# Kernel tuning notes

Hardware: AMD Instinct MI355X
Metric: run time of the kernel (lower is better)

Reference implementation:

```python
import jax, jax.numpy as jnp
import numpy as np

N = 50000
E = 800000
D = 128


def _gcn_layer(x, row, col, ew, W, b, n):
    # PyG GCNConv (normalize=True, add_self_loops=True):
    # self-loops were already appended to row/col/ew by the caller.
    deg = jax.ops.segment_sum(ew, col, num_segments=n)          # [N]
    dis = jnp.where(deg > 0, jax.lax.rsqrt(jnp.maximum(deg, 1e-12)), 0.0)
    norm = dis[row] * ew * dis[col]                              # [E+N]
    h = x @ W                                                    # [N, D]
    msg = h[row] * norm[:, None]                                 # [E+N, D] gather-scale
    out = jax.ops.segment_sum(msg, col, num_segments=n)          # scatter-add
    return out + b


def setup_inputs() -> dict:
    key = jax.random.key(0)
    k1, k2, k3, k4, k5 = jax.random.split(key, 5)
    x = jax.random.normal(k1, (N, D), dtype=jnp.float32)
    edge_index = jax.random.randint(k2, (2, E), 0, N, dtype=jnp.int64)
    edge_weight = jax.random.uniform(k3, (E,), dtype=jnp.float32)
    s = 1.0 / np.sqrt(D)
    W1 = jax.random.uniform(k4, (D, D), minval=-s, maxval=s, dtype=jnp.float32)
    b1 = jnp.zeros((D,), dtype=jnp.float32)
    W2 = jax.random.uniform(k5, (D, D), minval=-s, maxval=s, dtype=jnp.float32)
    b2 = jnp.zeros((D,), dtype=jnp.float32)
    return {"x": x, "edge_index": edge_index, "edge_weight": edge_weight,
            "W1": W1, "b1": b1, "W2": W2, "b2": b2}


def reference(x, edge_index, edge_weight, W1, b1, W2, b2):
    n = x.shape[0]
    loop = jnp.arange(n, dtype=edge_index.dtype)
    row = jnp.concatenate([edge_index[0], loop])
    col = jnp.concatenate([edge_index[1], loop])
    ew = jnp.concatenate([edge_weight, jnp.ones((n,), dtype=edge_weight.dtype)])
    h = _gcn_layer(x, row, col, ew, W1, b1, n)
    h = jax.nn.relu(h)
    # F.dropout(training=self.training): identity in eval mode
    out = _gcn_layer(h, row, col, ew, W2, b2, n)
    return out
```

## Files before the change

### kernel.cpp

```cpp
#include <hip/hip_runtime.h>

#define NN 50000
#define NE 800000
#define DD 128

#define CAP 64
#define FIX_SCALE 16777216.0f
#define NWELEM 16384
#define GEMM_GRID ((NN + 127) / 128)

#define SHIFT2 7
#define BWID 128
#define NBUCK ((NN + BWID - 1) / BWID)
#define CAP2 2560
#define NB1 128
#define EPB ((NE + NB1 - 1) / NB1)

typedef __attribute__((ext_vector_type(8))) short short8;
typedef __attribute__((ext_vector_type(4))) float floatx4;
typedef __attribute__((ext_vector_type(4))) _Float16 half4;
typedef __attribute__((ext_vector_type(8))) _Float16 half8;


__device__ __forceinline__ void split_trunc(float x, short& hi, short& lo) {
    unsigned uh = __float_as_uint(x) >> 16;
    hi = (short)uh;
    float r = x - __uint_as_float(uh << 16);
    lo = (short)(__float_as_uint(r) >> 16);
}


__global__ void init_prep(unsigned* __restrict__ bcur,
                          const float* __restrict__ W1, const float* __restrict__ W2,
                          unsigned short* __restrict__ w1hi, unsigned short* __restrict__ w1lo,
                          unsigned short* __restrict__ w2hi, unsigned short* __restrict__ w2lo) {
    int t = blockIdx.x * blockDim.x + threadIdx.x;
    if (t < NBUCK) bcur[t] = 0u;
    int u = t - 512;
    if (u >= 0 && u < 2 * NWELEM) {
        int which = u >> 14;
        int idx = u & (NWELEM - 1);
        int k = idx >> 7, n = idx & 127;
        const float* W = which ? W2 : W1;
        unsigned short* whi = which ? w2hi : w1hi;
        unsigned short* wlo = which ? w2lo : w1lo;
        short h, l;
        split_trunc(W[idx], h, l);
        whi[n * DD + k] = (unsigned short)h;
        wlo[n * DD + k] = (unsigned short)l;
    }
}


template <bool RELU, bool SCALE, typename InT>
__device__ __forceinline__ void gemm_core(int bid, const InT* __restrict__ in,
                                          const unsigned short* __restrict__ whi,
                                          const unsigned short* __restrict__ wlo,
                                          const float* __restrict__ dis,
                                          _Float16* __restrict__ out) {
    int lane = threadIdx.x & 63;
    int wid = threadIdx.x >> 6;
    int cg = wid & 1;
    int rg = wid >> 1;
    int l16 = lane & 15;
    int quad = lane >> 4;
    int koff_base = quad * 8;

    short8 bhi[4][4], blo[4][4];
#pragma unroll
    for (int t = 0; t < 4; t++) {
        int n = cg * 64 + t * 16 + l16;
#pragma unroll
        for (int ks = 0; ks < 4; ks++) {
            int koff = ks * 32 + koff_base;
            bhi[t][ks] = *(const short8*)(whi + n * DD + koff);
            blo[t][ks] = *(const short8*)(wlo + n * DD + koff);
        }
    }

#pragma unroll
    for (int chunk = 0; chunk < 4; chunk++) {
        int base = bid * 128 + chunk * 32 + rg * 16;
        int m = base + l16;
        int mld = (m < NN) ? m : 0;
        const InT* xr = in + (size_t)mld * DD;

        short8 ahi[4], alo[4];
#pragma unroll
        for (int ks = 0; ks < 4; ks++) {
            int koff = ks * 32 + koff_base;
            float v[8];
            if constexpr (sizeof(InT) == 4) {
                float4 a0 = *(const float4*)(xr + koff);
                float4 a1 = *(const float4*)(xr + koff + 4);
                v[0] = a0.x; v[1] = a0.y; v[2] = a0.z; v[3] = a0.w;
                v[4] = a1.x; v[5] = a1.y; v[6] = a1.z; v[7] = a1.w;
            } else {
                half8 a = *(const half8*)(xr + koff);
#pragma unroll
                for (int j = 0; j < 8; j++) v[j] = (float)a[j];
            }
#pragma unroll
            for (int j = 0; j < 8; j++) {
                float xv = RELU ? fmaxf(v[j], 0.0f) : v[j];
                short h, l;
                split_trunc(xv, h, l);
                ahi[ks][j] = h;
                alo[ks][j] = l;
            }
        }

        floatx4 acc[4];
#pragma unroll
        for (int t = 0; t < 4; t++) acc[t] = (floatx4)(0.0f);

#pragma unroll
        for (int ks = 0; ks < 4; ks++) {
#pragma unroll
            for (int t = 0; t < 4; t++) {
                acc[t] = __builtin_amdgcn_mfma_f32_16x16x32_bf16(ahi[ks], bhi[t][ks], acc[t], 0, 0, 0);
                acc[t] = __builtin_amdgcn_mfma_f32_16x16x32_bf16(alo[ks], bhi[t][ks], acc[t], 0, 0, 0);
                acc[t] = __builtin_amdgcn_mfma_f32_16x16x32_bf16(ahi[ks], blo[t][ks], acc[t], 0, 0, 0);
            }
        }

#pragma unroll
        for (int r = 0; r < 4; r++) {
            int rowm = base + quad * 4 + r;
            if (rowm < NN) {
                float dsc = SCALE ? dis[rowm] : 1.0f;
                _Float16* o = out + (size_t)rowm * DD + cg * 64 + l16;
#pragma unroll
                for (int t = 0; t < 4; t++) o[t * 16] = (_Float16)(acc[t][r] * dsc);
            }
        }
    }
}


__device__ __forceinline__ void scatter_core(int bid, const int* __restrict__ row,
                                             const int* __restrict__ col,
                                             const float* __restrict__ ew,
                                             unsigned* __restrict__ bcur,
                                             uint2* __restrict__ staged) {
    __shared__ unsigned cnt1[NBUCK];
    __shared__ unsigned base1[NBUCK];

    for (int k = threadIdx.x; k < NBUCK; k += 256) cnt1[k] = 0u;
    __syncthreads();

    int e0 = bid * EPB;
    int e1 = min(e0 + EPB, NE);

    for (int e = e0 + (int)threadIdx.x; e < e1; e += 256) {
        atomicAdd(&cnt1[col[e] >> SHIFT2], 1u);
    }
    __syncthreads();

    for (int k = threadIdx.x; k < NBUCK; k += 256) {
        unsigned n = cnt1[k];
        base1[k] = n ? atomicAdd(&bcur[k], n) : 0u;
        cnt1[k] = 0u;
    }
    __syncthreads();

    for (int e = e0 + (int)threadIdx.x; e < e1; e += 256) {
        int c = col[e];
        int bk = c >> SHIFT2;
        unsigned r = base1[bk] + atomicAdd(&cnt1[bk], 1u);
        if (r >= CAP2) r = CAP2 - 1;
        uint2 p;
        p.x = (unsigned)row[e] | ((unsigned)(c & (BWID - 1)) << 16);
        p.y = __float_as_uint(ew[e]);
        staged[(size_t)bk * CAP2 + r] = p;
    }
}


__global__ __launch_bounds__(256) void gemm1_scatter(const float* __restrict__ x,
                                                     const unsigned short* __restrict__ w1hi,
                                                     const unsigned short* __restrict__ w1lo,
                                                     _Float16* __restrict__ g,
                                                     const int* __restrict__ row,
                                                     const int* __restrict__ col,
                                                     const float* __restrict__ ew,
                                                     unsigned* __restrict__ bcur,
                                                     uint2* __restrict__ staged) {
    if (blockIdx.x < NB1) {
        scatter_core(blockIdx.x, row, col, ew, bcur, staged);
    } else {
        gemm_core<false, false, float>(blockIdx.x - NB1, x, w1hi, w1lo, nullptr, g);
    }
}

__global__ __launch_bounds__(256, 2) void gemm2(const _Float16* __restrict__ in,
                                                const unsigned short* __restrict__ whi,
                                                const unsigned short* __restrict__ wlo,
                                                const float* __restrict__ dis,
                                                _Float16* __restrict__ out) {
    gemm_core<true, true, _Float16>(blockIdx.x, in, whi, wlo, dis, out);
}


__global__ __launch_bounds__(256) void bucket_place(const unsigned* __restrict__ bcur,
                                                    const uint2* __restrict__ staged,
                                                    uint2* __restrict__ epk,
                                                    float* __restrict__ dis,
                                                    int* __restrict__ endarr,
                                                    _Float16* __restrict__ g) {
    __shared__ unsigned cntN[BWID];
    __shared__ unsigned wfix[BWID];
    __shared__ float disS[BWID];

    int b = blockIdx.x;
    int node0 = b << SHIFT2;
    int nn = min(BWID, NN - node0);

    if (threadIdx.x < BWID) { cntN[threadIdx.x] = 0u; wfix[threadIdx.x] = 0u; }
    __syncthreads();

    int m = min((int)bcur[b], CAP2);
    const uint2* st = staged + (size_t)b * CAP2;

    for (int j = threadIdx.x; j < m; j += 256) {
        uint2 p = st[j];
        int ln = (p.x >> 16) & (BWID - 1);
        atomicAdd(&cntN[ln], 1u);
        float w = __uint_as_float(p.y);
        atomicAdd(&wfix[ln], (unsigned)(w * FIX_SCALE + 0.5f));
    }
    __syncthreads();

    if (threadIdx.x < (unsigned)nn) {
        int i = node0 + threadIdx.x;
        float deg = 1.0f + (float)wfix[threadIdx.x] * (1.0f / FIX_SCALE);
        float d = rsqrtf(deg);
        disS[threadIdx.x] = d;
        dis[i] = d;
        endarr[i] = (i << 6) + min((int)cntN[threadIdx.x], CAP);
        cntN[threadIdx.x] = 0u;
    }
    __syncthreads();

    for (int j = threadIdx.x; j < m; j += 256) {
        uint2 p = st[j];
        int ln = (p.x >> 16) & (BWID - 1);
        unsigned r = atomicAdd(&cntN[ln], 1u);
        if (r < CAP) {
            int c = node0 + ln;
            uint2 q;
            q.x = (p.x & 0xFFFFu) << 7;
            q.y = p.y;
            epk[(c << 6) + (int)r] = q;
        }
    }

    half8* gb = (half8*)(g + (size_t)node0 * DD);
    for (int idx = threadIdx.x; idx < nn * 16; idx += 256) {
        float d = disS[idx >> 4];
        half8 hv = gb[idx];
#pragma unroll
        for (int jj = 0; jj < 8; jj++) hv[jj] = (_Float16)((float)hv[jj] * d);
        gb[idx] = hv;
    }
}


template <typename OutT>
__global__ __launch_bounds__(256) void agg_half(const int* __restrict__ endarr,
                                                const uint2* __restrict__ epk,
                                                const _Float16* __restrict__ g,
                                                const float* __restrict__ dis,
                                                const float* __restrict__ bias,
                                                OutT* __restrict__ out) {
    int i = (blockIdx.x * blockDim.x + threadIdx.x) >> 6;
    int lane = threadIdx.x & 63;
    int s = lane & 31;
    int half = lane >> 5;
    if (i >= NN) return;

    half4 gv = *(const half4*)(g + (size_t)i * DD + s * 4);
    float4 bb = ((const float4*)bias)[s];
    float d = dis[i];

    float ax = 0.0f, ay = 0.0f, az = 0.0f, aw = 0.0f;

    int start = i << 6;
    int end = endarr[i];
    int j = start + half;
    for (; j + 6 < end; j += 8) {
        uint2 p0 = epk[j], p1 = epk[j + 2], p2 = epk[j + 4], p3 = epk[j + 6];
        half4 v0 = *(const half4*)(g + p0.x + s * 4);
        half4 v1 = *(const half4*)(g + p1.x + s * 4);
        half4 v2 = *(const half4*)(g + p2.x + s * 4);
        half4 v3 = *(const half4*)(g + p3.x + s * 4);
        float n0 = __uint_as_float(p0.y), n1 = __uint_as_float(p1.y);
        float n2 = __uint_as_float(p2.y), n3 = __uint_as_float(p3.y);
        ax = fmaf(n0, (float)v0.x, ax); ay = fmaf(n0, (float)v0.y, ay);
        az = fmaf(n0, (float)v0.z, az); aw = fmaf(n0, (float)v0.w, aw);
        ax = fmaf(n1, (float)v1.x, ax); ay = fmaf(n1, (float)v1.y, ay);
        az = fmaf(n1, (float)v1.z, az); aw = fmaf(n1, (float)v1.w, aw);
        ax = fmaf(n2, (float)v2.x, ax); ay = fmaf(n2, (float)v2.y, ay);
        az = fmaf(n2, (float)v2.z, az); aw = fmaf(n2, (float)v2.w, aw);
        ax = fmaf(n3, (float)v3.x, ax); ay = fmaf(n3, (float)v3.y, ay);
        az = fmaf(n3, (float)v3.z, az); aw = fmaf(n3, (float)v3.w, aw);
    }
    for (; j < end; j += 2) {
        uint2 p = epk[j];
        float nm = __uint_as_float(p.y);
        half4 v = *(const half4*)(g + p.x + s * 4);
        ax = fmaf(nm, (float)v.x, ax); ay = fmaf(nm, (float)v.y, ay);
        az = fmaf(nm, (float)v.z, az); aw = fmaf(nm, (float)v.w, aw);
    }

    ax += __shfl_xor(ax, 32);
    ay += __shfl_xor(ay, 32);
    az += __shfl_xor(az, 32);
    aw += __shfl_xor(aw, 32);

    if (half == 0) {
        float ox = bb.x + d * (ax + (float)gv.x);
        float oy = bb.y + d * (ay + (float)gv.y);
        float oz = bb.z + d * (az + (float)gv.z);
        float ow = bb.w + d * (aw + (float)gv.w);
        if constexpr (sizeof(OutT) == 2) {
            half4 o;
            o.x = (_Float16)ox; o.y = (_Float16)oy;
            o.z = (_Float16)oz; o.w = (_Float16)ow;
            *(half4*)(out + (size_t)i * DD + s * 4) = o;
        } else {
            float4 o;
            o.x = ox; o.y = oy; o.z = oz; o.w = ow;
            ((float4*)(out + (size_t)i * DD))[s] = o;
        }
    }
}


extern "C" void kernel_launch(void* const* d_in, const int* in_sizes, int n_in,
                              void* d_out, int out_size, void* d_ws, size_t ws_size,
                              hipStream_t stream) {
    const float* x  = (const float*)d_in[0];
    const int*   ei = (const int*)d_in[1];
    const float* ew = (const float*)d_in[2];
    const float* W1 = (const float*)d_in[3];
    const float* b1 = (const float*)d_in[4];
    const float* W2 = (const float*)d_in[5];
    const float* b2 = (const float*)d_in[6];
    float* out = (float*)d_out;

    float* ws      = (float*)d_ws;
    float* dis     = ws;
    int*   endarr  = (int*)(ws + 50000);
    unsigned* bcur = (unsigned*)(ws + 100000);
    uint2* epk     = (uint2*)(ws + 900000);
    _Float16* gbuf = (_Float16*)(ws + 7300000);
    unsigned short* wt1hi = (unsigned short*)(ws + 10500000);
    unsigned short* wt1lo = (unsigned short*)(ws + 10508192);
    unsigned short* wt2hi = (unsigned short*)(ws + 10516384);
    unsigned short* wt2lo = (unsigned short*)(ws + 10524576);
    _Float16* out1 = (_Float16*)(ws + 10532768);
    uint2* staged  = (uint2*)(ws + 10532768);

    const int* rowi = ei;
    const int* coli = ei + NE;

    init_prep<<<(512 + 2 * NWELEM + 255) / 256, 256, 0, stream>>>(
        bcur, W1, W2, wt1hi, wt1lo, wt2hi, wt2lo);

    gemm1_scatter<<<NB1 + GEMM_GRID, 256, 0, stream>>>(
        x, wt1hi, wt1lo, gbuf, rowi, coli, ew, bcur, staged);

    bucket_place<<<NBUCK, 256, 0, stream>>>(bcur, staged, epk, dis, endarr, gbuf);

    const int agg_grid = (NN * 64) / 256 + 1;

    agg_half<_Float16><<<agg_grid, 256, 0, stream>>>(endarr, epk, gbuf, dis, b1, out1);

    gemm2<<<GEMM_GRID, 256, 0, stream>>>(out1, wt2hi, wt2lo, dis, gbuf);

    agg_half<float><<<agg_grid, 256, 0, stream>>>(endarr, epk, gbuf, dis, b2, out);
}
```

Before: 224.6 us.

## Replace global atomic bucket reservation with histogram pass and per-bucket prefix scan

The edge-bucketing step now runs a separate per-block histogram kernel (fused with the weight split), then a per-bucket prefix scan over blocks, so the scatter blocks get deterministic offsets without global atomics or a second counting pass. The number of scatter blocks is raised from 128 to 512 to spread the edge work. In exchange it adds an extra kernel launch and rereads the column array, and the bucket placement becomes deterministic.

```diff
diff --git a/kernel.cpp b/kernel.cpp
--- a/kernel.cpp
+++ b/kernel.cpp
@@ -13,8 +13,9 @@
 #define BWID 128
 #define NBUCK ((NN + BWID - 1) / BWID)
 #define CAP2 2560
-#define NB1 128
+#define NB1 512
 #define EPB ((NE + NB1 - 1) / NB1)
+#define NBK_PAD 392
 
 typedef __attribute__((ext_vector_type(8))) short short8;
 typedef __attribute__((ext_vector_type(4))) float floatx4;
@@ -30,14 +31,25 @@
 }
 
 
-__global__ void init_prep(unsigned* __restrict__ bcur,
-                          const float* __restrict__ W1, const float* __restrict__ W2,
-                          unsigned short* __restrict__ w1hi, unsigned short* __restrict__ w1lo,
-                          unsigned short* __restrict__ w2hi, unsigned short* __restrict__ w2lo) {
-    int t = blockIdx.x * blockDim.x + threadIdx.x;
-    if (t < NBUCK) bcur[t] = 0u;
-    int u = t - 512;
-    if (u >= 0 && u < 2 * NWELEM) {
+__global__ __launch_bounds__(256) void init_hist(const int* __restrict__ col,
+                                                 unsigned* __restrict__ hist,
+                                                 const float* __restrict__ W1, const float* __restrict__ W2,
+                                                 unsigned short* __restrict__ w1hi, unsigned short* __restrict__ w1lo,
+                                                 unsigned short* __restrict__ w2hi, unsigned short* __restrict__ w2lo) {
+    if (blockIdx.x < NB1) {
+        __shared__ unsigned h[NBUCK];
+        for (int k = threadIdx.x; k < NBUCK; k += 256) h[k] = 0u;
+        __syncthreads();
+        int e0 = blockIdx.x * EPB;
+        int e1 = min(e0 + EPB, NE);
+        for (int e = e0 + (int)threadIdx.x; e < e1; e += 256) {
+            atomicAdd(&h[col[e] >> SHIFT2], 1u);
+        }
+        __syncthreads();
+        unsigned* hb = hist + (size_t)blockIdx.x * NBK_PAD;
+        for (int k = threadIdx.x; k < NBUCK; k += 256) hb[k] = h[k];
+    } else {
+        int u = (blockIdx.x - NB1) * 256 + threadIdx.x;
         int which = u >> 14;
         int idx = u & (NWELEM - 1);
         int k = idx >> 7, n = idx & 127;
@@ -49,6 +61,29 @@
         whi[n * DD + k] = (unsigned short)h;
         wlo[n * DD + k] = (unsigned short)l;
     }
+}
+
+
+__global__ __launch_bounds__(NB1) void bucket_prefix(const unsigned* __restrict__ hist,
+                                                     unsigned* __restrict__ offs_t,
+                                                     unsigned* __restrict__ bcur) {
+    __shared__ unsigned sa[NB1], sb[NB1];
+    int k = blockIdx.x;
+    int t = threadIdx.x;
+    unsigned v = hist[(size_t)t * NBK_PAD + k];
+    sa[t] = v;
+    __syncthreads();
+    unsigned* src = sa;
+    unsigned* dst = sb;
+    for (int d = 1; d < NB1; d <<= 1) {
+        unsigned x = src[t] + (t >= d ? src[t - d] : 0u);
+        dst[t] = x;
+        __syncthreads();
+        unsigned* tmp = src; src = dst; dst = tmp;
+    }
+    unsigned inc = src[t];
+    offs_t[(size_t)k * NB1 + t] = inc - v;
+    if (t == NB1 - 1) bcur[k] = inc;
 }
 
 
@@ -141,38 +176,29 @@
 __device__ __forceinline__ void scatter_core(int bid, const int* __restrict__ row,
                                              const int* __restrict__ col,
                                              const float* __restrict__ ew,
-                                             unsigned* __restrict__ bcur,
+                                             const unsigned* __restrict__ offs_t,
                                              uint2* __restrict__ staged) {
+    __shared__ unsigned base1[NBUCK];
     __shared__ unsigned cnt1[NBUCK];
-    __shared__ unsigned base1[NBUCK];
-
-    for (int k = threadIdx.x; k < NBUCK; k += 256) cnt1[k] = 0u;
+
+    for (int k = threadIdx.x; k < NBUCK; k += 256) {
+        base1[k] = (unsigned)k * CAP2 + offs_t[(size_t)k * NB1 + bid];
+        cnt1[k] = 0u;
+    }
     __syncthreads();
 
     int e0 = bid * EPB;
     int e1 = min(e0 + EPB, NE);
-
-    for (int e = e0 + (int)threadIdx.x; e < e1; e += 256) {
-        atomicAdd(&cnt1[col[e] >> SHIFT2], 1u);
-    }
-    __syncthreads();
-
-    for (int k = threadIdx.x; k < NBUCK; k += 256) {
-        unsigned n = cnt1[k];
-        base1[k] = n ? atomicAdd(&bcur[k], n) : 0u;
-        cnt1[k] = 0u;
-    }
-    __syncthreads();
-
     for (int e = e0 + (int)threadIdx.x; e < e1; e += 256) {
         int c = col[e];
         int bk = c >> SHIFT2;
         unsigned r = base1[bk] + atomicAdd(&cnt1[bk], 1u);
-        if (r >= CAP2) r = CAP2 - 1;
+        unsigned lim = (unsigned)bk * CAP2 + (CAP2 - 1);
+        if (r > lim) r = lim;
         uint2 p;
         p.x = (unsigned)row[e] | ((unsigned)(c & (BWID - 1)) << 16);
         p.y = __float_as_uint(ew[e]);
-        staged[(size_t)bk * CAP2 + r] = p;
+        staged[r] = p;
     }
 }
 
@@ -184,10 +210,10 @@
                                                      const int* __restrict__ row,
                                                      const int* __restrict__ col,
                                                      const float* __restrict__ ew,
-                                                     unsigned* __restrict__ bcur,
+                                                     const unsigned* __restrict__ offs_t,
                                                      uint2* __restrict__ staged) {
     if (blockIdx.x < NB1) {
-        scatter_core(blockIdx.x, row, col, ew, bcur, staged);
+        scatter_core(blockIdx.x, row, col, ew, offs_t, staged);
     } else {
         gemm_core<false, false, float>(blockIdx.x - NB1, x, w1hi, w1lo, nullptr, g);
     }
@@ -353,6 +379,8 @@
     float* dis     = ws;
     int*   endarr  = (int*)(ws + 50000);
     unsigned* bcur = (unsigned*)(ws + 100000);
+    unsigned* hist = (unsigned*)(ws + 150000);
+    unsigned* offs_t = (unsigned*)(ws + 400000);
     uint2* epk     = (uint2*)(ws + 900000);
     _Float16* gbuf = (_Float16*)(ws + 7300000);
     unsigned short* wt1hi = (unsigned short*)(ws + 10500000);
@@ -365,11 +393,13 @@
     const int* rowi = ei;
     const int* coli = ei + NE;
 
-    init_prep<<<(512 + 2 * NWELEM + 255) / 256, 256, 0, stream>>>(
-        bcur, W1, W2, wt1hi, wt1lo, wt2hi, wt2lo);
+    init_hist<<<NB1 + (2 * NWELEM) / 256, 256, 0, stream>>>(
+        coli, hist, W1, W2, wt1hi, wt1lo, wt2hi, wt2lo);
+
+    bucket_prefix<<<NBUCK, NB1, 0, stream>>>(hist, offs_t, bcur);
 
     gemm1_scatter<<<NB1 + GEMM_GRID, 256, 0, stream>>>(
-        x, wt1hi, wt1lo, gbuf, rowi, coli, ew, bcur, staged);
+        x, wt1hi, wt1lo, gbuf, rowi, coli, ew, offs_t, staged);
 
     bucket_place<<<NBUCK, 256, 0, stream>>>(bcur, staged, epk, dis, endarr, gbuf);
 
```

New measurement: 227.2 us. About the same (+1.2%).
